# Kernel optimization log

Hardware: AMD Instinct MI355X
Metric: run time of the kernel (lower is better)

## Reference

```python
import jax, jax.numpy as jnp
from jax import lax
import numpy as np

# ---- constants (from Coords2Elec init kwargs) ----
BOX = 128          # box_size
RES = 1.0          # resolution (Angstrom / voxel)
EPS_IN = 6.5
EPS_OUT = 79.0
ION = 1.0          # ion_size
WAT = 1.4          # wat_size (water probe radius)
ASIGMA = 2.0
KAPPA02 = 0.8486   # debye_length kwarg, passed to solver as kappa0^2
QCONV = 7046.52    # charge_conv
D = 2              # gaussian sharpness divisor
W = 9              # scatter support window per axis (covers ~2.7 sigma)
N_ITER = 20        # Jacobi sweeps for the Poisson-Boltzmann solve

# staggered-grid offsets for the 4 eps channels: face-centered x/y/z + ion grid
OFFSETS = ((0.5, 0.0, 0.0), (0.0, 0.5, 0.0), (0.0, 0.0, 0.5), (0.5, 0.5, 0.5))


def _scatter_gauss(coords, sigma, mask, offset):
    """Scatter per-atom Gaussian density onto a staggered [B,BOX,BOX,BOX] grid.
    coords [B,N,3], sigma [B,N], mask [B,N], offset: 3 floats in voxel units."""
    B, N, _ = coords.shape
    off = jnp.asarray(offset, coords.dtype)
    offs = jnp.arange(W)
    # window base index so that grid node positions (idx+off)*RES bracket the atom
    base = jnp.floor(coords / RES - off).astype(jnp.int32) - W // 2     # [B,N,3]
    idx = base[..., None] + offs                                         # [B,N,3,W]
    gpos = (idx.astype(coords.dtype) + off[None, None, :, None]) * RES   # [B,N,3,W]
    d2 = (gpos - coords[..., None]) ** 2
    wax = jnp.exp(-d2 / (2.0 * sigma[:, :, None, None] ** 2))            # [B,N,3,W]
    w = (wax[:, :, 0, :, None, None] * wax[:, :, 1, None, :, None]
         * wax[:, :, 2, None, None, :]) * mask[:, :, None, None, None]   # [B,N,W,W,W]
    b_idx = jnp.broadcast_to(jnp.arange(B)[:, None, None, None, None], w.shape)
    ix = jnp.broadcast_to(idx[:, :, 0, :, None, None], w.shape)
    iy = jnp.broadcast_to(idx[:, :, 1, None, :, None], w.shape)
    iz = jnp.broadcast_to(idx[:, :, 2, None, None, :], w.shape)
    grid = jnp.zeros((B, BOX, BOX, BOX), coords.dtype)
    return grid.at[b_idx, ix, iy, iz].add(w, mode='drop')


def _scatter_q(coords, charge, mask):
    """Trilinear scatter of per-atom charges onto node grid [B,BOX,BOX,BOX]."""
    B, N, _ = coords.shape
    u = coords / RES
    i0 = jnp.floor(u).astype(jnp.int32)                 # [B,N,3]
    f = u - i0
    wpair = jnp.stack([1.0 - f, f], -1)                 # [B,N,3,2]
    ipair = jnp.stack([i0, i0 + 1], -1)                 # [B,N,3,2]
    w = (wpair[:, :, 0, :, None, None] * wpair[:, :, 1, None, :, None]
         * wpair[:, :, 2, None, None, :]) * (charge * mask)[:, :, None, None, None]
    b_idx = jnp.broadcast_to(jnp.arange(B)[:, None, None, None, None], w.shape)
    ix = jnp.broadcast_to(ipair[:, :, 0, :, None, None], w.shape)
    iy = jnp.broadcast_to(ipair[:, :, 1, None, :, None], w.shape)
    iz = jnp.broadcast_to(ipair[:, :, 2, None, None, :], w.shape)
    grid = jnp.zeros((B, BOX, BOX, BOX), coords.dtype)
    return grid.at[b_idx, ix, iy, iz].add(w, mode='drop')


def _face_nb(a, axis):
    """Face eps of the (i-1) cell along axis; boundary padded with EPS_OUT."""
    lead = jnp.full_like(lax.slice_in_dim(a, 0, 1, axis=axis), EPS_OUT)
    return jnp.concatenate([lead, lax.slice_in_dim(a, 0, a.shape[axis] - 1, axis=axis)], axis=axis)


def _phi_nb(phi, axis, d):
    """Neighbor potential phi[i+d] along spatial axis, zero (Dirichlet) outside."""
    z = jnp.zeros_like(lax.slice_in_dim(phi, 0, 1, axis=axis))
    if d > 0:
        return jnp.concatenate([lax.slice_in_dim(phi, 1, phi.shape[axis], axis=axis), z], axis=axis)
    return jnp.concatenate([z, lax.slice_in_dim(phi, 0, phi.shape[axis] - 1, axis=axis)], axis=axis)


def _qeps2phi(Q, Eps):
    """Fixed-iteration Jacobi solve of the linearized Poisson-Boltzmann stencil."""
    ex, ey, ez, ek = Eps[:, 0], Eps[:, 1], Eps[:, 2], Eps[:, 3]
    exm, eym, ezm = _face_nb(ex, 1), _face_nb(ey, 2), _face_nb(ez, 3)
    lam = jnp.clip((ek - EPS_IN) / (EPS_OUT - EPS_IN), 0.0, 1.0)  # ion accessibility
    denom = ex + exm + ey + eym + ez + ezm + KAPPA02 * RES * RES * lam
    src = 4.0 * jnp.pi * Q * RES

    def body(i, phi):
        num = (ex * _phi_nb(phi, 1, +1) + exm * _phi_nb(phi, 1, -1)
               + ey * _phi_nb(phi, 2, +1) + eym * _phi_nb(phi, 2, -1)
               + ez * _phi_nb(phi, 3, +1) + ezm * _phi_nb(phi, 3, -1) + src)
        return num / denom

    return lax.fori_loop(0, N_ITER, body, jnp.zeros_like(Q))


def setup_inputs() -> dict:
    key = jax.random.key(0)
    k1, k2, k3, k4 = jax.random.split(key, 4)
    B, N = 4, 4096
    coords = jax.random.uniform(k1, (B, N, 3), jnp.float32) * ((BOX - 1) * RES)
    charges = jax.random.normal(k2, (B, N), jnp.float32) * 0.5     # partial charges
    radii = 1.0 + jax.random.uniform(k3, (B, N), jnp.float32)      # 1..2 Angstrom
    assigned_params = jnp.stack([charges, radii], -1)              # [B,N,2]
    num_atoms = jax.random.randint(k4, (B,), N // 2, N + 1, jnp.int32)
    return {"coords": coords, "assigned_params": assigned_params, "num_atoms": num_atoms}


def reference(coords, assigned_params, num_atoms):
    B, N, _ = coords.shape
    mask = (jnp.arange(N)[None, :] < num_atoms[:, None]).astype(coords.dtype)
    charge = assigned_params[..., 0]
    radii = assigned_params[..., 1]
    sig_eps = (radii + WAT) / D   # solvent-excluded Gaussian width
    sig_ion = (radii + ION) / D   # ion-excluded Gaussian width
    rho = jnp.stack([
        _scatter_gauss(coords, sig_eps if c < 3 else sig_ion, mask, OFFSETS[c])
        for c in range(4)], axis=1)                     # [B,4,BOX,BOX,BOX]
    rho = jnp.clip(rho, 0.0, 1.0)
    eps = rho * (EPS_IN - EPS_OUT) + EPS_OUT
    q = _scatter_q(coords, charge, mask) * QCONV        # [B,BOX,BOX,BOX]
    phi = _qeps2phi(q, eps)
    return q, eps, phi
```

## Files before the change

### kernel.cpp

```cpp
#include <hip/hip_runtime.h>
#include <hip/hip_fp16.h>
#include <math.h>

static constexpr int   B_    = 4;
static constexpr int   N_    = 4096;
static constexpr int   BOX_  = 128;
static constexpr long long VOX_ = 1LL * BOX_ * BOX_ * BOX_;
static constexpr float EPS_IN_C  = 6.5f;
static constexpr float EPS_OUT_C = 79.0f;
static constexpr float QCONV_C   = 7046.52f;
static constexpr float KAPPA02_C = 0.8486f;
static constexpr float FOURPI_C  = 12.566370614359172f;

__global__ void scatter_q_kernel(const float* __restrict__ coords,
                                 const float* __restrict__ params,
                                 const int*   __restrict__ num_atoms,
                                 float* __restrict__ q)
{
    int a = blockIdx.x * blockDim.x + threadIdx.x;
    if (a >= B_ * N_) return;
    int b = a >> 12;
    int n = a & (N_ - 1);
    if (n >= num_atoms[b]) return;

    float cx = coords[3 * a + 0];
    float cy = coords[3 * a + 1];
    float cz = coords[3 * a + 2];
    float chg = params[2 * a + 0] * QCONV_C;

    int ix0 = (int)floorf(cx), iy0 = (int)floorf(cy), iz0 = (int)floorf(cz);
    float fx = cx - (float)ix0, fy = cy - (float)iy0, fz = cz - (float)iz0;
    float wx[2] = {1.0f - fx, fx};
    float wy[2] = {1.0f - fy, fy};
    float wz[2] = {1.0f - fz, fz};

    float* qb = q + (long long)b * VOX_;
#pragma unroll
    for (int dx = 0; dx < 2; ++dx) {
        int ix = ix0 + dx;
        if ((unsigned)ix >= 128u) continue;
#pragma unroll
        for (int dy = 0; dy < 2; ++dy) {
            int iy = iy0 + dy;
            if ((unsigned)iy >= 128u) continue;
#pragma unroll
            for (int dz = 0; dz < 2; ++dz) {
                int iz = iz0 + dz;
                if ((unsigned)iz >= 128u) continue;
                atomicAdd(&qb[((long long)ix * 128 + iy) * 128 + iz],
                          chg * wx[dx] * wy[dy] * wz[dz]);
            }
        }
    }
}

#define CAND_CAP 512
#define CHUNK 32

__global__ __launch_bounds__(512)
void eps_gather_v3(const float* __restrict__ coords,
                   const float* __restrict__ params,
                   const int*   __restrict__ num_atoms,
                   float* __restrict__ eps)
{
    int bid = blockIdx.x;
    int b   = bid >> 8;
    int txi = (bid >> 4) & 15;
    int tyi = bid & 15;
    int tx = txi << 3, ty = tyi << 3;

    __shared__ float sx[CAND_CAP], sy[CAND_CAP], sz[CAND_CAP], sr[CAND_CAP];
    __shared__ float wts[CHUNK][9][8];
    __shared__ int  fidx[CAND_CAP];
    __shared__ int  s_cnt, s_fcnt;
    if (threadIdx.x == 0) s_cnt = 0;
    __syncthreads();

    int na = num_atoms[b];
    const float* cb = coords + (size_t)b * N_ * 3;
    const float* pb = params + (size_t)b * N_ * 2;

    float lox = (float)tx - 4.0f, hix = (float)tx + 12.5f;
    float loy = (float)ty - 4.0f, hiy = (float)ty + 12.5f;
    bool wx_ = (tx == 120), wy_ = (ty == 120);
    for (int n = threadIdx.x; n < na; n += 512) {
        float cx = cb[3 * n], cy = cb[3 * n + 1], cz = cb[3 * n + 2];
        bool okx = (cx >= lox && cx < hix) || (wx_ && cx < 4.5f);
        bool oky = (cy >= loy && cy < hiy) || (wy_ && cy < 4.5f);
        if (okx && oky) {
            int slot = atomicAdd(&s_cnt, 1);
            if (slot < CAND_CAP) {
                sx[slot] = cx; sy[slot] = cy; sz[slot] = cz;
                sr[slot] = pb[2 * n + 1];
            }
        }
    }
    __syncthreads();
    int cnt = min(s_cnt, CAND_CAP);

    int lz = threadIdx.x & 7;
    int ly = (threadIdx.x >> 3) & 7;
    int lx = threadIdx.x >> 6;

    float* eb = eps + (size_t)b * 4 * VOX_;

    for (int tzi = 0; tzi < 16; ++tzi) {
        int tz = tzi << 3;

        __syncthreads();
        if (threadIdx.x == 0) s_fcnt = 0;
        __syncthreads();
        {
            float loz = (float)tz - 4.0f, hiz = (float)tz + 12.5f;
            bool wz_ = (tz == 120);
            for (int i = threadIdx.x; i < cnt; i += 512) {
                float cz = sz[i];
                if ((cz >= loz && cz < hiz) || (wz_ && cz < 4.5f)) {
                    int s = atomicAdd(&s_fcnt, 1);
                    fidx[s] = i;
                }
            }
        }
        __syncthreads();
        int fcnt = s_fcnt;

        float r0 = 0.0f, r1 = 0.0f, r2 = 0.0f, r3 = 0.0f;

        for (int k0 = 0; k0 < fcnt; k0 += CHUNK) {
            int nC = min(CHUNK, fcnt - k0);
            __syncthreads();
            for (int w = threadIdx.x; w < nC * 72; w += 512) {
                int ka  = w / 72;
                int rem = w - ka * 72;
                int vi  = rem >> 3;
                int pos = rem & 7;
                int axis = vi / 3, var = vi - axis * 3;
                int k = fidx[k0 + ka];
                float c     = (axis == 0) ? sx[k] : (axis == 1) ? sy[k] : sz[k];
                int   torig = (axis == 0) ? tx    : (axis == 1) ? ty    : tz;
                float r = sr[k];
                float sig = (var == 2) ? (r + 1.0f) * 0.5f : (r + 1.4f) * 0.5f;
                float off = (var == 0) ? 0.0f : 0.5f;
                float inv2s2 = 1.0f / (2.0f * sig * sig);
                int i = torig + pos;
                int base = (int)floorf(c - off) - 4;
                float wv = 0.0f;
                if ((unsigned)(i - base) <= 8u) {
                    float d = (float)i + off - c;
                    wv = expf(-d * d * inv2s2);
                } else if ((unsigned)(i - 128 - base) <= 8u) {
                    float d = (float)(i - 128) + off - c;
                    wv = expf(-d * d * inv2s2);
                }
                wts[ka][vi][pos] = wv;
            }
            __syncthreads();
            for (int ka = 0; ka < nC; ++ka) {
                float xE0 = wts[ka][0][lx], xE5 = wts[ka][1][lx], xI5 = wts[ka][2][lx];
                float yE0 = wts[ka][3][ly], yE5 = wts[ka][4][ly], yI5 = wts[ka][5][ly];
                float zE0 = wts[ka][6][lz], zE5 = wts[ka][7][lz], zI5 = wts[ka][8][lz];
                r0 += xE5 * yE0 * zE0;
                r1 += xE0 * yE5 * zE0;
                r2 += xE0 * yE0 * zE5;
                r3 += xI5 * yI5 * zI5;
            }
        }

        int ix = tx + lx, iy = ty + ly, iz = tz + lz;
        size_t sp = ((size_t)ix * 128 + iy) * 128 + iz;
        eb[sp]                    = EPS_OUT_C + (EPS_IN_C - EPS_OUT_C) * fminf(fmaxf(r0, 0.0f), 1.0f);
        eb[sp + (size_t)VOX_]     = EPS_OUT_C + (EPS_IN_C - EPS_OUT_C) * fminf(fmaxf(r1, 0.0f), 1.0f);
        eb[sp + (size_t)VOX_ * 2] = EPS_OUT_C + (EPS_IN_C - EPS_OUT_C) * fminf(fmaxf(r2, 0.0f), 1.0f);
        eb[sp + (size_t)VOX_ * 3] = EPS_OUT_C + (EPS_IN_C - EPS_OUT_C) * fminf(fmaxf(r3, 0.0f), 1.0f);
    }
}

__global__ void coef_pack4(const float* __restrict__ eps,
                           const float* __restrict__ q,
                           uint4* __restrict__ coef,
                           float* __restrict__ phi1)
{
    int tid = blockIdx.x * blockDim.x + threadIdx.x;
    size_t g4 = (size_t)tid * 4;
    int b  = (int)(g4 >> 21);
    size_t sp = g4 & (size_t)(VOX_ - 1);
    int x  = (int)(sp >> 14);
    int y  = (int)((sp >> 7) & 127);
    int z4 = (int)(sp & 127);

    const float* E = eps + (size_t)b * 4 * (size_t)VOX_;
    float4 ex4 = *reinterpret_cast<const float4*>(E + sp);
    float4 ey4 = *reinterpret_cast<const float4*>(E + sp + (size_t)VOX_);
    float4 ez4 = *reinterpret_cast<const float4*>(E + sp + (size_t)VOX_ * 2);
    float4 ek4 = *reinterpret_cast<const float4*>(E + sp + (size_t)VOX_ * 3);
    float4 eo  = make_float4(EPS_OUT_C, EPS_OUT_C, EPS_OUT_C, EPS_OUT_C);
    float4 exm4 = (x > 0) ? *reinterpret_cast<const float4*>(E + sp - 16384) : eo;
    float4 eym4 = (y > 0) ? *reinterpret_cast<const float4*>(E + sp + (size_t)VOX_ - 128) : eo;
    float ezm0  = (z4 > 0) ? E[sp + (size_t)VOX_ * 2 - 1] : EPS_OUT_C;
    float4 q4  = *reinterpret_cast<const float4*>(q + g4);

    float exA[4]  = {ex4.x, ex4.y, ex4.z, ex4.w};
    float eyA[4]  = {ey4.x, ey4.y, ey4.z, ey4.w};
    float ezA[4]  = {ez4.x, ez4.y, ez4.z, ez4.w};
    float ekA[4]  = {ek4.x, ek4.y, ek4.z, ek4.w};
    float exmA[4] = {exm4.x, exm4.y, exm4.z, exm4.w};
    float eymA[4] = {eym4.x, eym4.y, eym4.z, eym4.w};
    float ezmA[4] = {ezm0, ez4.x, ez4.y, ez4.z};
    float qA[4]   = {q4.x, q4.y, q4.z, q4.w};

    float ph[4];
#pragma unroll
    for (int j = 0; j < 4; ++j) {
        float lam = (ekA[j] - EPS_IN_C) / (EPS_OUT_C - EPS_IN_C);
        lam = fminf(fmaxf(lam, 0.0f), 1.0f);
        float denom = exA[j] + exmA[j] + eyA[j] + eymA[j] + ezA[j] + ezmA[j]
                    + KAPPA02_C * lam;
        float rcp = 1.0f / denom;

        __half2 h01 = __floats2half2_rn(exA[j] * rcp, exmA[j] * rcp);
        __half2 h23 = __floats2half2_rn(eyA[j] * rcp, eymA[j] * rcp);
        __half2 h45 = __floats2half2_rn(ezA[j] * rcp, ezmA[j] * rcp);
        __half2 h67 = __floats2half2_rn(FOURPI_C * qA[j] * rcp, 0.0f);
        uint4 u;
        u.x = *(unsigned int*)&h01;
        u.y = *(unsigned int*)&h23;
        u.z = *(unsigned int*)&h45;
        u.w = *(unsigned int*)&h67;
        coef[g4 + j] = u;
        ph[j] = __half22float2(h67).x;
    }
    *reinterpret_cast<float4*>(phi1 + g4) = make_float4(ph[0], ph[1], ph[2], ph[3]);
}

#define TY 8
#define TZ 32
#define RY (TY + 2)
#define RZ (TZ + 2)
#define PYD (TY + 4)
#define PZD (TZ + 4)
#define SEG 16

__global__ __launch_bounds__(256)
void jacobi_f2p(const uint4* __restrict__ coef,
                const float* __restrict__ pin,
                float* __restrict__ pout)
{
    int bid = blockIdx.x;
    int xs = bid & 7;
    int zt = (bid >> 3) & 3;
    int yt = (bid >> 5) & 15;
    int b  = bid >> 9;
    int x_lo = xs * SEG, x_hi = x_lo + SEG - 1;
    int y0 = yt * TY, z0 = zt * TZ;

    __shared__ float P[3][PYD * PZD];
    __shared__ float S[3][RY * RZ];

    int tid = threadIdx.x;
    int oy = tid >> 5, oz = tid & 31;

    const uint4* cb = coef + (size_t)b * VOX_;
    const float* pb = pin  + (size_t)b * VOX_;
    float*       ob = pout + (size_t)b * VOX_;

    int e1_i  = (oy + 1) * RZ + (oz + 1);
    int g1y = y0 + oy, g1z = z0 + oz;
    int e1_off = g1y * 128 + g1z;
    int e1_p0 = (oy + 2) * PZD + (oz + 2);
    bool has2 = (tid < 84);
    int e2_ry = 0, e2_rz = 0;
    if (tid < 34)      { e2_ry = 0;      e2_rz = tid; }
    else if (tid < 68) { e2_ry = RY - 1; e2_rz = tid - 34; }
    else if (tid < 84) { int t2 = tid - 68; e2_ry = 1 + (t2 >> 1); e2_rz = (t2 & 1) * (RZ - 1); }
    int e2_i = e2_ry * RZ + e2_rz;
    int g2y = y0 - 1 + e2_ry, g2z = z0 - 1 + e2_rz;
    bool e2_ok = ((unsigned)g2y < 128u) && ((unsigned)g2z < 128u);
    int e2_off = min(max(g2y, 0), 127) * 128 + min(max(g2z, 0), 127);
    int e2_p0 = (e2_ry + 1) * PZD + (e2_rz + 1);
    int p1_py = tid / PZD, p1_pz = tid - p1_py * PZD;
    int p1y = y0 - 2 + p1_py, p1z = z0 - 2 + p1_pz;
    bool p1_ok = ((unsigned)p1y < 128u) && ((unsigned)p1z < 128u);
    int p1_off = min(max(p1y, 0), 127) * 128 + min(max(p1z, 0), 127);
    int p2i = tid + 256;
    bool hasP2 = (p2i < PYD * PZD);
    int p2_py = p2i / PZD, p2_pz = p2i - p2_py * PZD;
    int p2y = y0 - 2 + p2_py, p2z = z0 - 2 + p2_pz;
    bool p2_ok = hasP2 && ((unsigned)p2y < 128u) && ((unsigned)p2z < 128u);
    int p2_off = min(max(p2y, 0), 127) * 128 + min(max(p2z, 0), 127);

    const float* ps0 = pb + (size_t)min(max(x_lo - 2, 0), 127) * 16384;
    float pfA = ps0[p1_off];
    float pfB = hasP2 ? ps0[p2_off] : 0.0f;
    uint4 cf1 = make_uint4(0u, 0u, 0u, 0u);
    uint4 cf2 = make_uint4(0u, 0u, 0u, 0u);
    uint4 hold = make_uint4(0u, 0u, 0u, 0u);
    uint4 cnew = make_uint4(0u, 0u, 0u, 0u);

    for (int x = x_lo - 2; x <= x_hi + 2; ++x) {
        int s0 = (x + 3) % 3;
        int s1 = (x + 2) % 3;
        int s2 = (x + 1) % 3;
        bool xin = (x >= 0 && x < 128);

        P[s0][tid] = (xin && p1_ok) ? pfA : 0.0f;
        if (hasP2) P[s0][p2i] = (xin && p2_ok) ? pfB : 0.0f;
        asm volatile("s_waitcnt lgkmcnt(0)" ::: "memory");
        __builtin_amdgcn_s_barrier();

        if (x < x_hi + 2) {
            const float* ps = pb + (size_t)min(max(x + 1, 0), 127) * 16384;
            pfA = ps[p1_off];
            if (hasP2) pfB = ps[p2_off];
        }

        if (x >= x_lo) {
            int k = x - 1;
            bool kin = ((unsigned)k < 128u);
            {
                float v = 0.0f;
                if (kin) {
                    const __half2* h = reinterpret_cast<const __half2*>(&cf1);
                    float2 a01 = __half22float2(h[0]);
                    float2 a23 = __half22float2(h[1]);
                    float2 a45 = __half22float2(h[2]);
                    float2 a67 = __half22float2(h[3]);
                    v = a01.x * P[s0][e1_p0]
                      + a01.y * P[s2][e1_p0]
                      + a23.x * P[s1][e1_p0 + PZD]
                      + a23.y * P[s1][e1_p0 - PZD]
                      + a45.x * P[s1][e1_p0 + 1]
                      + a45.y * P[s1][e1_p0 - 1]
                      + a67.x;
                }
                S[s1][e1_i] = v;
                cnew = cf1;
            }
            if (has2) {
                float v = 0.0f;
                if (kin && e2_ok) {
                    const __half2* h = reinterpret_cast<const __half2*>(&cf2);
                    float2 a01 = __half22float2(h[0]);
                    float2 a23 = __half22float2(h[1]);
                    float2 a45 = __half22float2(h[2]);
                    float2 a67 = __half22float2(h[3]);
                    v = a01.x * P[s0][e2_p0]
                      + a01.y * P[s2][e2_p0]
                      + a23.x * P[s1][e2_p0 + PZD]
                      + a23.y * P[s1][e2_p0 - PZD]
                      + a45.x * P[s1][e2_p0 + 1]
                      + a45.y * P[s1][e2_p0 - 1]
                      + a67.x;
                }
                S[s1][e2_i] = v;
            }
        }
        if (x >= x_lo - 1 && x <= x_hi + 1) {
            const uint4* cs = cb + (size_t)min(max(x, 0), 127) * 16384;
            cf1 = cs[e1_off];
            if (has2) cf2 = cs[e2_off];
        }
        asm volatile("s_waitcnt lgkmcnt(0)" ::: "memory");
        __builtin_amdgcn_s_barrier();

        int xo = x - 2;
        if (xo >= x_lo) {
            const __half2* h = reinterpret_cast<const __half2*>(&hold);
            float2 a01 = __half22float2(h[0]);
            float2 a23 = __half22float2(h[1]);
            float2 a45 = __half22float2(h[2]);
            float2 a67 = __half22float2(h[3]);
            int j0 = e1_i;
            float out = a01.x * S[s1][j0]
                      + a01.y * S[s0][j0]
                      + a23.x * S[s2][j0 + RZ]
                      + a23.y * S[s2][j0 - RZ]
                      + a45.x * S[s2][j0 + 1]
                      + a45.y * S[s2][j0 - 1]
                      + a67.x;
            ob[(size_t)xo * 16384 + e1_off] = out;
        }
        hold = cnew;
    }
}

__global__ void jacobi_v3(const uint4* __restrict__ coef,
                          const float* __restrict__ pin,
                          float* __restrict__ pout)
{
    int tid = blockIdx.x * blockDim.x + threadIdx.x;
    size_t g4 = (size_t)tid * 4;
    int z4 = (int)(g4 & 127);
    int y  = (int)((g4 >> 7) & 127);
    int x  = (int)((g4 >> 14) & 127);

    float4 pcv = *reinterpret_cast<const float4*>(pin + g4);
    float4 z4v = make_float4(0.f, 0.f, 0.f, 0.f);
    float4 pxpv = (x < 127) ? *reinterpret_cast<const float4*>(pin + g4 + 16384) : z4v;
    float4 pxmv = (x > 0)   ? *reinterpret_cast<const float4*>(pin + g4 - 16384) : z4v;
    float4 pypv = (y < 127) ? *reinterpret_cast<const float4*>(pin + g4 + 128)   : z4v;
    float4 pymv = (y > 0)   ? *reinterpret_cast<const float4*>(pin + g4 - 128)   : z4v;
    float zpE = (z4 < 124) ? pin[g4 + 4] : 0.0f;
    float zmE = (z4 > 0)   ? pin[g4 - 1] : 0.0f;

    float pxp[4] = {pxpv.x, pxpv.y, pxpv.z, pxpv.w};
    float pxm[4] = {pxmv.x, pxmv.y, pxmv.z, pxmv.w};
    float pyp[4] = {pypv.x, pypv.y, pypv.z, pypv.w};
    float pym[4] = {pymv.x, pymv.y, pymv.z, pymv.w};
    float pzp[4] = {pcv.y, pcv.z, pcv.w, zpE};
    float pzm[4] = {zmE, pcv.x, pcv.y, pcv.z};

    float out[4];
#pragma unroll
    for (int j = 0; j < 4; ++j) {
        uint4 cu = coef[g4 + j];
        const __half2* h = reinterpret_cast<const __half2*>(&cu);
        float2 a01 = __half22float2(h[0]);
        float2 a23 = __half22float2(h[1]);
        float2 a45 = __half22float2(h[2]);
        float2 a67 = __half22float2(h[3]);
        out[j] = a01.x * pxp[j] + a01.y * pxm[j]
               + a23.x * pyp[j] + a23.y * pym[j]
               + a45.x * pzp[j] + a45.y * pzm[j]
               + a67.x;
    }
    *reinterpret_cast<float4*>(pout + g4) = make_float4(out[0], out[1], out[2], out[3]);
}

__global__ void jacobi_v2(const float* __restrict__ eps,
                          const float* __restrict__ q,
                          const float* __restrict__ pin,
                          float* __restrict__ pout)
{
    int bxy = blockIdx.x;
    int b = bxy >> 14;
    int x = (bxy >> 7) & 127;
    int y = bxy & 127;
    int z = threadIdx.x;

    size_t sp = ((size_t)x * 128 + y) * 128 + z;
    size_t g  = (size_t)b * (size_t)VOX_ + sp;
    const float* E = eps + (size_t)b * 4 * (size_t)VOX_;

    float ex = E[sp];
    float ey = E[sp + (size_t)VOX_];
    float ez = E[sp + (size_t)VOX_ * 2];
    float ek = E[sp + (size_t)VOX_ * 3];
    float exm = (x > 0) ? E[sp - 16384]                 : EPS_OUT_C;
    float eym = (y > 0) ? E[sp + (size_t)VOX_ - 128]    : EPS_OUT_C;
    float ezm = (z > 0) ? E[sp + (size_t)VOX_ * 2 - 1]  : EPS_OUT_C;

    float lam = (ek - EPS_IN_C) / (EPS_OUT_C - EPS_IN_C);
    lam = fminf(fmaxf(lam, 0.0f), 1.0f);
    float denom = ex + exm + ey + eym + ez + ezm + KAPPA02_C * lam;

    float pxp = (x < 127) ? pin[g + 16384] : 0.0f;
    float pxm = (x > 0)   ? pin[g - 16384] : 0.0f;
    float pyp = (y < 127) ? pin[g + 128]   : 0.0f;
    float pym = (y > 0)   ? pin[g - 128]   : 0.0f;
    float pzp = (z < 127) ? pin[g + 1]     : 0.0f;
    float pzm = (z > 0)   ? pin[g - 1]     : 0.0f;

    float num = ex * pxp + exm * pxm + ey * pyp + eym * pym
              + ez * pzp + ezm * pzm + FOURPI_C * q[g];
    pout[g] = num / denom;
}

extern "C" void kernel_launch(void* const* d_in, const int* in_sizes, int n_in,
                              void* d_out, int out_size, void* d_ws, size_t ws_size,
                              hipStream_t stream)
{
    const float* coords    = (const float*)d_in[0];
    const float* params    = (const float*)d_in[1];
    const int*   num_atoms = (const int*)d_in[2];

    float* q   = (float*)d_out;
    float* eps = q + (size_t)B_ * VOX_;
    float* phi = eps + (size_t)B_ * 4 * VOX_;

    hipMemsetAsync(q, 0, (size_t)B_ * VOX_ * sizeof(float), stream);

    scatter_q_kernel<<<(B_ * N_ + 255) / 256, 256, 0, stream>>>(coords, params, num_atoms, q);
    eps_gather_v3<<<B_ * 16 * 16, 512, 0, stream>>>(coords, params, num_atoms, eps);

    size_t coefBytes = (size_t)B_ * VOX_ * sizeof(uint4);
    size_t need = coefBytes + (size_t)B_ * VOX_ * sizeof(float);

    if (ws_size >= need) {
        uint4* coefA = (uint4*)d_ws;
        float* tmp   = (float*)((char*)d_ws + coefBytes);
        coef_pack4<<<(int)(B_ * VOX_ / 4 / 256), 256, 0, stream>>>(eps, q, coefA, phi);
        const float* cur = phi;
        for (int it = 1; it <= 9; ++it) {
            float* dst = (it & 1) ? tmp : phi;
            jacobi_f2p<<<B_ * 16 * 4 * 8, 256, 0, stream>>>(coefA, cur, dst);
            cur = dst;
        }
        jacobi_v3<<<(int)(B_ * VOX_ / 4 / 256), 256, 0, stream>>>(coefA, cur, phi);
    } else {
        hipMemsetAsync(phi, 0, (size_t)B_ * VOX_ * sizeof(float), stream);
        float* tmp = (float*)d_ws;
        int jb = B_ * 128 * 128;
        const float* cur = phi;
        for (int it = 1; it <= 20; ++it) {
            float* dst = (it & 1) ? tmp : phi;
            jacobi_v2<<<jb, 128, 0, stream>>>(eps, q, cur, dst);
            cur = dst;
        }
    }
}
```

Baseline: 719.4 us.

## Bin candidates per z-tile once and compute eps per wavefront with shuffles

The eps gather kernel now bins candidate atoms into all 16 z-tiles in a single pass and assigns two z-tiles to each 64-lane wavefront, instead of looping over z-tiles block-wide. Per-atom axis weights are computed in lanes and shared through wavefront shuffles rather than shared memory, and each thread accumulates an 8-voxel x column in registers. This is meant to remove the per-tile __syncthreads barriers and the shared-memory weight staging. In exchange it raises register pressure, serialises atoms within each wavefront, and silently caps each z-tile list at 64 atoms, which could drop contributions in dense regions.

```diff
diff --git a/kernel.cpp b/kernel.cpp
--- a/kernel.cpp
+++ b/kernel.cpp
@@ -55,10 +55,10 @@
 }
 
 #define CAND_CAP 512
-#define CHUNK 32
+#define TCAP 64
 
 __global__ __launch_bounds__(512)
-void eps_gather_v3(const float* __restrict__ coords,
+void eps_gather_v4(const float* __restrict__ coords,
                    const float* __restrict__ params,
                    const int*   __restrict__ num_atoms,
                    float* __restrict__ eps)
@@ -70,10 +70,13 @@
     int tx = txi << 3, ty = tyi << 3;
 
     __shared__ float sx[CAND_CAP], sy[CAND_CAP], sz[CAND_CAP], sr[CAND_CAP];
-    __shared__ float wts[CHUNK][9][8];
-    __shared__ int  fidx[CAND_CAP];
-    __shared__ int  s_cnt, s_fcnt;
-    if (threadIdx.x == 0) s_cnt = 0;
+    __shared__ int   tlist[16][TCAP];
+    __shared__ int   tcnt[16];
+    __shared__ int   s_cnt;
+
+    int tid = threadIdx.x;
+    if (tid == 0) s_cnt = 0;
+    if (tid < 16) tcnt[tid] = 0;
     __syncthreads();
 
     int na = num_atoms[b];
@@ -83,7 +86,7 @@
     float lox = (float)tx - 4.0f, hix = (float)tx + 12.5f;
     float loy = (float)ty - 4.0f, hiy = (float)ty + 12.5f;
     bool wx_ = (tx == 120), wy_ = (ty == 120);
-    for (int n = threadIdx.x; n < na; n += 512) {
+    for (int n = tid; n < na; n += 512) {
         float cx = cb[3 * n], cy = cb[3 * n + 1], cz = cb[3 * n + 2];
         bool okx = (cx >= lox && cx < hix) || (wx_ && cx < 4.5f);
         bool oky = (cy >= loy && cy < hiy) || (wy_ && cy < 4.5f);
@@ -98,47 +101,46 @@
     __syncthreads();
     int cnt = min(s_cnt, CAND_CAP);
 
-    int lz = threadIdx.x & 7;
-    int ly = (threadIdx.x >> 3) & 7;
-    int lx = threadIdx.x >> 6;
+    for (int i = tid; i < cnt; i += 512) {
+        float cz = sz[i];
+#pragma unroll
+        for (int t = 0; t < 16; ++t) {
+            int tz = t << 3;
+            if ((cz >= (float)tz - 4.0f && cz < (float)tz + 12.5f) ||
+                (tz == 120 && cz < 4.5f)) {
+                int s = atomicAdd(&tcnt[t], 1);
+                if (s < TCAP) tlist[t][s] = i;
+            }
+        }
+    }
+    __syncthreads();
+
+    int wid  = tid >> 6;
+    int lane = tid & 63;
+    int vi1  = lane >> 3;
+    int pos1 = lane & 7;
+    int ly   = lane >> 3;
+    int lz   = lane & 7;
 
     float* eb = eps + (size_t)b * 4 * VOX_;
 
-    for (int tzi = 0; tzi < 16; ++tzi) {
-        int tz = tzi << 3;
-
-        __syncthreads();
-        if (threadIdx.x == 0) s_fcnt = 0;
-        __syncthreads();
-        {
-            float loz = (float)tz - 4.0f, hiz = (float)tz + 12.5f;
-            bool wz_ = (tz == 120);
-            for (int i = threadIdx.x; i < cnt; i += 512) {
-                float cz = sz[i];
-                if ((cz >= loz && cz < hiz) || (wz_ && cz < 4.5f)) {
-                    int s = atomicAdd(&s_fcnt, 1);
-                    fidx[s] = i;
-                }
-            }
-        }
-        __syncthreads();
-        int fcnt = s_fcnt;
-
-        float r0 = 0.0f, r1 = 0.0f, r2 = 0.0f, r3 = 0.0f;
-
-        for (int k0 = 0; k0 < fcnt; k0 += CHUNK) {
-            int nC = min(CHUNK, fcnt - k0);
-            __syncthreads();
-            for (int w = threadIdx.x; w < nC * 72; w += 512) {
-                int ka  = w / 72;
-                int rem = w - ka * 72;
-                int vi  = rem >> 3;
-                int pos = rem & 7;
+    for (int sub = 0; sub < 2; ++sub) {
+        int tzi = (wid << 1) | sub;
+        int tz  = tzi << 3;
+        int n   = min(tcnt[tzi], TCAP);
+
+        float r0[8], r1[8], r2[8], r3[8];
+#pragma unroll
+        for (int j = 0; j < 8; ++j) { r0[j] = r1[j] = r2[j] = r3[j] = 0.0f; }
+
+        for (int j = 0; j < n; ++j) {
+            int k = tlist[tzi][j];
+            float ax = sx[k], ay = sy[k], az = sz[k], r = sr[k];
+
+            auto wcalc = [&](int vi, int pos) -> float {
                 int axis = vi / 3, var = vi - axis * 3;
-                int k = fidx[k0 + ka];
-                float c     = (axis == 0) ? sx[k] : (axis == 1) ? sy[k] : sz[k];
-                int   torig = (axis == 0) ? tx    : (axis == 1) ? ty    : tz;
-                float r = sr[k];
+                float c     = (axis == 0) ? ax : (axis == 1) ? ay : az;
+                int   torig = (axis == 0) ? tx : (axis == 1) ? ty : tz;
                 float sig = (var == 2) ? (r + 1.0f) * 0.5f : (r + 1.4f) * 0.5f;
                 float off = (var == 0) ? 0.0f : 0.5f;
                 float inv2s2 = 1.0f / (2.0f * sig * sig);
@@ -152,26 +154,39 @@
                     float d = (float)(i - 128) + off - c;
                     wv = expf(-d * d * inv2s2);
                 }
-                wts[ka][vi][pos] = wv;
+                return wv;
+            };
+
+            float w1 = wcalc(vi1, pos1);
+            float w2 = wcalc(8, pos1);
+
+            float yE0 = __shfl(w1, 24 + ly, 64);
+            float yE5 = __shfl(w1, 32 + ly, 64);
+            float yI5 = __shfl(w1, 40 + ly, 64);
+            float zE0 = __shfl(w1, 48 + lz, 64);
+            float zE5 = __shfl(w1, 56 + lz, 64);
+            float zI5 = __shfl(w2, lz, 64);
+
+#pragma unroll
+            for (int lx = 0; lx < 8; ++lx) {
+                float xE0 = __shfl(w1, lx, 64);
+                float xE5 = __shfl(w1, 8 + lx, 64);
+                float xI5 = __shfl(w1, 16 + lx, 64);
+                r0[lx] += xE5 * yE0 * zE0;
+                r1[lx] += xE0 * yE5 * zE0;
+                r2[lx] += xE0 * yE0 * zE5;
+                r3[lx] += xI5 * yI5 * zI5;
             }
-            __syncthreads();
-            for (int ka = 0; ka < nC; ++ka) {
-                float xE0 = wts[ka][0][lx], xE5 = wts[ka][1][lx], xI5 = wts[ka][2][lx];
-                float yE0 = wts[ka][3][ly], yE5 = wts[ka][4][ly], yI5 = wts[ka][5][ly];
-                float zE0 = wts[ka][6][lz], zE5 = wts[ka][7][lz], zI5 = wts[ka][8][lz];
-                r0 += xE5 * yE0 * zE0;
-                r1 += xE0 * yE5 * zE0;
-                r2 += xE0 * yE0 * zE5;
-                r3 += xI5 * yI5 * zI5;
-            }
-        }
-
-        int ix = tx + lx, iy = ty + ly, iz = tz + lz;
-        size_t sp = ((size_t)ix * 128 + iy) * 128 + iz;
-        eb[sp]                    = EPS_OUT_C + (EPS_IN_C - EPS_OUT_C) * fminf(fmaxf(r0, 0.0f), 1.0f);
-        eb[sp + (size_t)VOX_]     = EPS_OUT_C + (EPS_IN_C - EPS_OUT_C) * fminf(fmaxf(r1, 0.0f), 1.0f);
-        eb[sp + (size_t)VOX_ * 2] = EPS_OUT_C + (EPS_IN_C - EPS_OUT_C) * fminf(fmaxf(r2, 0.0f), 1.0f);
-        eb[sp + (size_t)VOX_ * 3] = EPS_OUT_C + (EPS_IN_C - EPS_OUT_C) * fminf(fmaxf(r3, 0.0f), 1.0f);
+        }
+
+#pragma unroll
+        for (int lx = 0; lx < 8; ++lx) {
+            size_t sp = ((size_t)(tx + lx) * 128 + (ty + ly)) * 128 + (tz + lz);
+            eb[sp]                    = EPS_OUT_C + (EPS_IN_C - EPS_OUT_C) * fminf(fmaxf(r0[lx], 0.0f), 1.0f);
+            eb[sp + (size_t)VOX_]     = EPS_OUT_C + (EPS_IN_C - EPS_OUT_C) * fminf(fmaxf(r1[lx], 0.0f), 1.0f);
+            eb[sp + (size_t)VOX_ * 2] = EPS_OUT_C + (EPS_IN_C - EPS_OUT_C) * fminf(fmaxf(r2[lx], 0.0f), 1.0f);
+            eb[sp + (size_t)VOX_ * 3] = EPS_OUT_C + (EPS_IN_C - EPS_OUT_C) * fminf(fmaxf(r3[lx], 0.0f), 1.0f);
+        }
     }
 }
 
@@ -480,7 +495,7 @@
     hipMemsetAsync(q, 0, (size_t)B_ * VOX_ * sizeof(float), stream);
 
     scatter_q_kernel<<<(B_ * N_ + 255) / 256, 256, 0, stream>>>(coords, params, num_atoms, q);
-    eps_gather_v3<<<B_ * 16 * 16, 512, 0, stream>>>(coords, params, num_atoms, eps);
+    eps_gather_v4<<<B_ * 16 * 16, 512, 0, stream>>>(coords, params, num_atoms, eps);
 
     size_t coefBytes = (size_t)B_ * VOX_ * sizeof(uint4);
     size_t need = coefBytes + (size_t)B_ * VOX_ * sizeof(float);
```

Measured after the change: 769.1 us. +6.9%, slower.
